# Performance work log

Measured on AMD Instinct MI355X. Metric: run time of the kernel, lower is better.

The kernel has to match this reference:

```python
import jax, jax.numpy as jnp
import numpy as np

N_NODES = 100000
DEG = 16          # regular-graph degree so degrees[start] > 0 for all nodes
STEPS = 32
D_FEAT = 16
MAXI32 = 2147483647


def setup_inputs() -> dict:
    key = jax.random.key(0)
    k1, k2, k3 = jax.random.split(key, 3)
    x = jax.random.normal(k1, (N_NODES, D_FEAT), dtype=jnp.float32)
    # CSR-style flat adjacency list: node v's neighbors are
    # adj_nodes[adj_offset[v] : adj_offset[v] + degrees[v]]
    adj_nodes = jax.random.randint(k2, (N_NODES * DEG,), 0, N_NODES, dtype=jnp.int32)
    adj_offset = (jnp.arange(N_NODES, dtype=jnp.int32) * DEG)
    degrees = jnp.full((N_NODES,), DEG, dtype=jnp.int32)
    # cache of random integers, one per (step, walk), as in the torch code
    choices = jax.random.randint(k3, (STEPS, N_NODES), 0, MAXI32, dtype=jnp.int32)
    return {"x": x, "adj_nodes": adj_nodes, "adj_offset": adj_offset,
            "degrees": degrees, "choices": choices}


def reference(x, adj_nodes, adj_offset, degrees, choices):
    """Non-backtracking random walk (Walker.sample_walks with start_p=1.0,
    all nodes having degree > 0, so start = arange(n)).
    Returns walks [steps+1, w] and walk_edges [steps, w]."""
    n = degrees.shape[0]
    nb_degrees = jnp.maximum(degrees - 1, 1)  # reduced degree for non-backtrack rewrite
    start = jnp.arange(n, dtype=jnp.int32)

    def step(carry, ch):
        prev, cur = carry                      # [w] previous / current nodes
        deg = degrees[cur]
        edge_idx = ch % deg                    # unweighted modulo edge choice
        chosen = adj_offset[cur] + edge_idx
        new = adj_nodes[chosen]
        bt = new == prev                       # backtracking walks
        # conditional rewrite: pick a different outgoing edge
        alt = adj_offset[cur] + (edge_idx + 1 + ch % nb_degrees[cur]) % deg
        chosen = jnp.where(bt, alt, chosen)
        new = jnp.where(bt, adj_nodes[alt], new)
        return (cur, new), (new, chosen)

    # prev = -1 at step 0 => bt is all-False, matching the i > 0 guard
    prev0 = jnp.full_like(start, -1)
    _, (nodes, walk_edges) = jax.lax.scan(step, (prev0, start), choices)
    walks = jnp.concatenate([start[None, :], nodes], axis=0)  # [steps+1, w]
    return walks, walk_edges
```

## Files before the change

### kernel.cpp

```cpp
#include <hip/hip_runtime.h>


#define DEG 16
#define CHAINS 2
#define NMAX 131072
#define PACK_BLOCK 256

__device__ unsigned int g_pk32[(size_t)NMAX * 9];
__device__ int g_flag;

__global__ __launch_bounds__(PACK_BLOCK) void pack_check_kernel(
    const int* __restrict__ adj_nodes,
    const int* __restrict__ adj_offset,
    const int* __restrict__ degrees,
    int n) {
    __shared__ __align__(16) unsigned int lds[PACK_BLOCK * 9];

    int tid = threadIdx.x;
    int blockStart = blockIdx.x * PACK_BLOCK;
    int v = blockStart + tid;

    bool bad = false;
    if (v < n) {
        bad = (degrees[v] != DEG) || (adj_offset[v] != v * DEG);

        const uint4* row4 = (const uint4*)(adj_nodes + (size_t)v * DEG);
        uint4 r[4];
        r[0] = row4[0]; r[1] = row4[1]; r[2] = row4[2]; r[3] = row4[3];
        const unsigned* rr = (const unsigned*)r;

        unsigned hbits = 0;
#pragma unroll
        for (int j = 0; j < 8; ++j) {
            unsigned u0 = rr[2 * j];
            unsigned u1 = rr[2 * j + 1];
            if (u0 >= 131072u || u1 >= 131072u) bad = true;
            lds[tid * 9 + j] = (u0 & 0xffffu) | ((u1 & 0xffffu) << 16);
            hbits |= ((u0 >> 16) & 1u) << (2 * j);
            hbits |= ((u1 >> 16) & 1u) << (2 * j + 1);
        }
        lds[tid * 9 + 8] = hbits;
    }
    __syncthreads();

    int rows = n - blockStart;
    if (rows > PACK_BLOCK) rows = PACK_BLOCK;
    unsigned int* dstBase = g_pk32 + (size_t)blockStart * 9;
    if (rows == PACK_BLOCK) {
        uint4* dst4 = (uint4*)dstBase;
        const uint4* src4 = (const uint4*)lds;
        for (int i = tid; i < (PACK_BLOCK * 9) / 4; i += PACK_BLOCK)
            dst4[i] = src4[i];
    } else {
        int ndw = rows * 9;
        for (int i = tid; i < ndw; i += PACK_BLOCK) dstBase[i] = lds[i];
    }

    if (bad) atomicOr(&g_flag, 1);
}

template <int STEPS>
__global__ __launch_bounds__(64) void walker_fast2(
    const int* __restrict__ choices,
    int* __restrict__ out, int n, int h,
    const int* __restrict__ adj_nodes,
    const int* __restrict__ adj_offset,
    const int* __restrict__ degrees) {

    int t = blockIdx.x * blockDim.x + threadIdx.x;
    if (t >= h) return;

    const unsigned short* __restrict__ pk = (const unsigned short*)g_pk32;

    int* walks      = out;
    int* walk_edges = out + (STEPS + 1) * n;

    int w0 = t;
    int w1 = t + h;
    bool has1 = (w1 < n);
    int w1s = has1 ? w1 : w0;

    __builtin_nontemporal_store(w0, &walks[w0]);
    if (has1) __builtin_nontemporal_store(w1, &walks[w1]);

    if (g_flag == 0) {
        int c0[STEPS], c1[STEPS];
#pragma unroll
        for (int i = 0; i < STEPS; ++i) {
            c0[i] = __builtin_nontemporal_load(&choices[i * n + w0]);
            c1[i] = __builtin_nontemporal_load(&choices[i * n + w1s]);
        }

        int prev0 = -1, cur0 = w0;
        int prev1 = -1, cur1 = w1s;
#pragma unroll
        for (int i = 0; i < STEPS; ++i) {
            unsigned ch0 = (unsigned)c0[i];
            unsigned ch1 = (unsigned)c1[i];
            unsigned e0 = ch0 & (DEG - 1);
            unsigned e1 = ch1 & (DEG - 1);

            const unsigned short* r0 = pk + (unsigned)cur0 * 18u;
            const unsigned short* r1 = pk + (unsigned)cur1 * 18u;

            unsigned l00 = r0[e0];
            unsigned hb0 = r0[16];
            unsigned l10 = r1[e1];
            unsigned hb1 = r1[16];

            int n00 = (int)(l00 | (((hb0 >> e0) & 1u) << 16));
            int n10 = (int)(l10 | (((hb1 >> e1) & 1u) << 16));

            int nw0 = n00, nw1 = n10;
            unsigned ef0 = e0, ef1 = e1;
            if (n00 == prev0) {
                unsigned a0 = (e0 + 1u + ch0 % (DEG - 1)) & (DEG - 1);
                unsigned l01 = r0[a0];
                nw0 = (int)(l01 | (((hb0 >> a0) & 1u) << 16));
                ef0 = a0;
            }
            if (n10 == prev1) {
                unsigned a1 = (e1 + 1u + ch1 % (DEG - 1)) & (DEG - 1);
                unsigned l11 = r1[a1];
                nw1 = (int)(l11 | (((hb1 >> a1) & 1u) << 16));
                ef1 = a1;
            }

            int ce0 = (cur0 << 4) + (int)ef0;
            int ce1 = (cur1 << 4) + (int)ef1;

            __builtin_nontemporal_store(nw0, &walks[(i + 1) * n + w0]);
            __builtin_nontemporal_store(ce0, &walk_edges[i * n + w0]);
            if (has1) {
                __builtin_nontemporal_store(nw1, &walks[(i + 1) * n + w1]);
                __builtin_nontemporal_store(ce1, &walk_edges[i * n + w1]);
            }
            prev0 = cur0; cur0 = nw0;
            prev1 = cur1; cur1 = nw1;
        }
    } else {
        for (int k = 0; k < 2; ++k) {
            int w = (k == 0) ? w0 : w1;
            if (w >= n) break;
            int prev = -1, cur = w;
            for (int i = 0; i < STEPS; ++i) {
                int chv = choices[i * n + w];
                int deg = degrees[cur];
                int off = adj_offset[cur];
                int nb  = deg - 1 > 1 ? deg - 1 : 1;

                int e      = chv % deg;
                int chosen = off + e;
                int alt    = off + (e + 1 + chv % nb) % deg;

                int nv0 = adj_nodes[chosen];
                int nv1 = adj_nodes[alt];

                bool bt = (nv0 == prev);
                int nw  = bt ? nv1 : nv0;
                walks[(i + 1) * n + w] = nw;
                walk_edges[i * n + w]  = bt ? alt : chosen;
                prev = cur;
                cur  = nw;
            }
        }
    }
}

__global__ __launch_bounds__(256) void walker_generic(
    const int* __restrict__ adj_nodes,
    const int* __restrict__ adj_offset,
    const int* __restrict__ degrees,
    const int* __restrict__ choices,
    int* __restrict__ out, int n, int steps) {

    int w = blockIdx.x * blockDim.x + threadIdx.x;
    if (w >= n) return;

    int* walks      = out;
    int* walk_edges = out + (steps + 1) * n;
    walks[w] = w;

    int prev = -1, cur = w;
    for (int i = 0; i < steps; ++i) {
        int chv = choices[i * n + w];
        int deg = degrees[cur];
        int off = adj_offset[cur];
        int nb  = deg - 1 > 1 ? deg - 1 : 1;

        int e      = chv % deg;
        int chosen = off + e;
        int alt    = off + (e + 1 + chv % nb) % deg;

        int nv0 = adj_nodes[chosen];
        int nv1 = adj_nodes[alt];

        bool bt = (nv0 == prev);
        int nw  = bt ? nv1 : nv0;
        walks[(i + 1) * n + w] = nw;
        walk_edges[i * n + w]  = bt ? alt : chosen;
        prev = cur;
        cur  = nw;
    }
}

extern "C" void kernel_launch(void* const* d_in, const int* in_sizes, int n_in,
                              void* d_out, int out_size, void* d_ws, size_t ws_size,
                              hipStream_t stream) {
    const int* adj_nodes  = (const int*)d_in[1];
    const int* adj_offset = (const int*)d_in[2];
    const int* degrees    = (const int*)d_in[3];
    const int* choices    = (const int*)d_in[4];
    int* out = (int*)d_out;

    int n     = in_sizes[2];
    int steps = in_sizes[4] / n;

    if (steps == 32 && n <= NMAX) {
        static int* flag_addr = nullptr;
        if (!flag_addr) {
            (void)hipGetSymbolAddress((void**)&flag_addr, HIP_SYMBOL(g_flag));
        }
        hipMemsetAsync(flag_addr, 0, sizeof(int), stream);

        int pg = (n + PACK_BLOCK - 1) / PACK_BLOCK;
        pack_check_kernel<<<pg, PACK_BLOCK, 0, stream>>>(adj_nodes, adj_offset,
                                                         degrees, n);
        int h  = (n + CHAINS - 1) / CHAINS;
        int wb = 64, wg = (h + wb - 1) / wb;
        walker_fast2<32><<<wg, wb, 0, stream>>>(choices, out, n, h,
                                                adj_nodes, adj_offset, degrees);
    } else {
        int block = 256, grid = (n + block - 1) / block;
        walker_generic<<<grid, block, 0, stream>>>(adj_nodes, adj_offset,
                                                   degrees, choices, out, n, steps);
    }
}
```

Measured before the change: 107.1 us.

## Pack adjacency as 18-bit fields and replace flag memset with epoch

Result: faster. 104.9 us (-2.0%).

```diff
diff --git a/kernel.cpp b/kernel.cpp
--- a/kernel.cpp
+++ b/kernel.cpp
@@ -5,15 +5,16 @@
 #define CHAINS 2
 #define NMAX 131072
 #define PACK_BLOCK 256
-
-__device__ unsigned int g_pk32[(size_t)NMAX * 9];
+#define ENT_MASK 0x3FFFFu
+
+__device__ unsigned int g_pk32[(size_t)NMAX * 9 + 2];
 __device__ int g_flag;
 
 __global__ __launch_bounds__(PACK_BLOCK) void pack_check_kernel(
     const int* __restrict__ adj_nodes,
     const int* __restrict__ adj_offset,
     const int* __restrict__ degrees,
-    int n) {
+    int n, int epoch) {
     __shared__ __align__(16) unsigned int lds[PACK_BLOCK * 9];
 
     int tid = threadIdx.x;
@@ -29,17 +30,21 @@
         r[0] = row4[0]; r[1] = row4[1]; r[2] = row4[2]; r[3] = row4[3];
         const unsigned* rr = (const unsigned*)r;
 
-        unsigned hbits = 0;
-#pragma unroll
-        for (int j = 0; j < 8; ++j) {
-            unsigned u0 = rr[2 * j];
-            unsigned u1 = rr[2 * j + 1];
-            if (u0 >= 131072u || u1 >= 131072u) bad = true;
-            lds[tid * 9 + j] = (u0 & 0xffffu) | ((u1 & 0xffffu) << 16);
-            hbits |= ((u0 >> 16) & 1u) << (2 * j);
-            hbits |= ((u1 >> 16) & 1u) << (2 * j + 1);
-        }
-        lds[tid * 9 + 8] = hbits;
+        unsigned dw[9];
+#pragma unroll
+        for (int j = 0; j < 9; ++j) dw[j] = 0u;
+#pragma unroll
+        for (int e = 0; e < 16; ++e) {
+            unsigned id = rr[e];
+            if (id >= 262144u) bad = true;
+            unsigned s   = 18u * (unsigned)e;
+            unsigned d   = s >> 5;
+            unsigned off = s & 31u;
+            dw[d] |= id << off;
+            if (off > 14u) dw[d + 1] |= id >> (32u - off);
+        }
+#pragma unroll
+        for (int j = 0; j < 9; ++j) lds[tid * 9 + j] = dw[j];
     }
     __syncthreads();
 
@@ -56,21 +61,37 @@
         for (int i = tid; i < ndw; i += PACK_BLOCK) dstBase[i] = lds[i];
     }
 
-    if (bad) atomicOr(&g_flag, 1);
+    if (bad) g_flag = epoch;
+}
+
+__global__ __launch_bounds__(256) void validate_kernel(
+    const int* __restrict__ adj_nodes, int n, int epoch) {
+    int v = blockIdx.x * blockDim.x + threadIdx.x;
+    if (v >= n) return;
+    const unsigned* row = g_pk32 + (size_t)v * 9;
+    bool bad = false;
+#pragma unroll
+    for (int e = 0; e < 16; ++e) {
+        unsigned s   = 18u * (unsigned)e;
+        unsigned d   = s >> 5;
+        unsigned off = s & 31u;
+        uint2 q = *(const uint2*)(row + d);
+        unsigned id = __builtin_amdgcn_alignbit(q.y, q.x, off) & ENT_MASK;
+        if (id != (unsigned)adj_nodes[(size_t)v * DEG + e]) bad = true;
+    }
+    if (bad) g_flag = epoch;
 }
 
 template <int STEPS>
-__global__ __launch_bounds__(64) void walker_fast2(
+__global__ __launch_bounds__(64) void walker_fast4(
     const int* __restrict__ choices,
-    int* __restrict__ out, int n, int h,
+    int* __restrict__ out, int n, int h, int epoch,
     const int* __restrict__ adj_nodes,
     const int* __restrict__ adj_offset,
     const int* __restrict__ degrees) {
 
     int t = blockIdx.x * blockDim.x + threadIdx.x;
     if (t >= h) return;
-
-    const unsigned short* __restrict__ pk = (const unsigned short*)g_pk32;
 
     int* walks      = out;
     int* walk_edges = out + (STEPS + 1) * n;
@@ -83,7 +104,7 @@
     __builtin_nontemporal_store(w0, &walks[w0]);
     if (has1) __builtin_nontemporal_store(w1, &walks[w1]);
 
-    if (g_flag == 0) {
+    if (g_flag != epoch) {
         int c0[STEPS], c1[STEPS];
 #pragma unroll
         for (int i = 0; i < STEPS; ++i) {
@@ -100,29 +121,32 @@
             unsigned e0 = ch0 & (DEG - 1);
             unsigned e1 = ch1 & (DEG - 1);
 
-            const unsigned short* r0 = pk + (unsigned)cur0 * 18u;
-            const unsigned short* r1 = pk + (unsigned)cur1 * 18u;
-
-            unsigned l00 = r0[e0];
-            unsigned hb0 = r0[16];
-            unsigned l10 = r1[e1];
-            unsigned hb1 = r1[16];
-
-            int n00 = (int)(l00 | (((hb0 >> e0) & 1u) << 16));
-            int n10 = (int)(l10 | (((hb1 >> e1) & 1u) << 16));
+            const unsigned* row0 = g_pk32 + (size_t)(unsigned)cur0 * 9u;
+            const unsigned* row1 = g_pk32 + (size_t)(unsigned)cur1 * 9u;
+
+            unsigned s0 = 18u * e0, d0 = s0 >> 5, f0 = s0 & 31u;
+            unsigned s1 = 18u * e1, d1 = s1 >> 5, f1 = s1 & 31u;
+
+            uint2 q0 = *(const uint2*)(row0 + d0);
+            uint2 q1 = *(const uint2*)(row1 + d1);
+
+            int n00 = (int)(__builtin_amdgcn_alignbit(q0.y, q0.x, f0) & ENT_MASK);
+            int n10 = (int)(__builtin_amdgcn_alignbit(q1.y, q1.x, f1) & ENT_MASK);
 
             int nw0 = n00, nw1 = n10;
             unsigned ef0 = e0, ef1 = e1;
             if (n00 == prev0) {
                 unsigned a0 = (e0 + 1u + ch0 % (DEG - 1)) & (DEG - 1);
-                unsigned l01 = r0[a0];
-                nw0 = (int)(l01 | (((hb0 >> a0) & 1u) << 16));
+                unsigned sa = 18u * a0, da = sa >> 5, fa = sa & 31u;
+                uint2 qa = *(const uint2*)(row0 + da);
+                nw0 = (int)(__builtin_amdgcn_alignbit(qa.y, qa.x, fa) & ENT_MASK);
                 ef0 = a0;
             }
             if (n10 == prev1) {
                 unsigned a1 = (e1 + 1u + ch1 % (DEG - 1)) & (DEG - 1);
-                unsigned l11 = r1[a1];
-                nw1 = (int)(l11 | (((hb1 >> a1) & 1u) << 16));
+                unsigned sb = 18u * a1, db = sb >> 5, fb = sb & 31u;
+                uint2 qb = *(const uint2*)(row1 + db);
+                nw1 = (int)(__builtin_amdgcn_alignbit(qb.y, qb.x, fb) & ENT_MASK);
                 ef1 = a1;
             }
 
@@ -217,18 +241,17 @@
     int steps = in_sizes[4] / n;
 
     if (steps == 32 && n <= NMAX) {
-        static int* flag_addr = nullptr;
-        if (!flag_addr) {
-            (void)hipGetSymbolAddress((void**)&flag_addr, HIP_SYMBOL(g_flag));
-        }
-        hipMemsetAsync(flag_addr, 0, sizeof(int), stream);
+        static int s_epoch = 0;
+        int epoch = ++s_epoch;
 
         int pg = (n + PACK_BLOCK - 1) / PACK_BLOCK;
         pack_check_kernel<<<pg, PACK_BLOCK, 0, stream>>>(adj_nodes, adj_offset,
-                                                         degrees, n);
+                                                         degrees, n, epoch);
+        validate_kernel<<<pg, PACK_BLOCK, 0, stream>>>(adj_nodes, n, epoch);
+
         int h  = (n + CHAINS - 1) / CHAINS;
         int wb = 64, wg = (h + wb - 1) / wb;
-        walker_fast2<32><<<wg, wb, 0, stream>>>(choices, out, n, h,
+        walker_fast4<32><<<wg, wb, 0, stream>>>(choices, out, n, h, epoch,
                                                 adj_nodes, adj_offset, degrees);
     } else {
         int block = 256, grid = (n + block - 1) / block;
```
